# Kernel optimization log

Hardware: AMD Instinct MI355X
Metric: run time of the kernel (lower is better)

Reference implementation:

```python
import jax, jax.numpy as jnp
import numpy as np

NUM_NODES = 100000
NUM_EDGES = 1600000
NUM_GRAPHS = 64
D_IN = 128
HID = 256
N_ATTR = 8
D_OUT = 1


def setup_inputs() -> dict:
    key = jax.random.key(0)
    ks = jax.random.split(key, 16)
    x = jax.random.normal(ks[0], (NUM_NODES, D_IN), dtype=jnp.float32)
    edge_index = jax.random.randint(ks[1], (2, NUM_EDGES), 0, NUM_NODES, dtype=jnp.int64)
    batch = jnp.sort(jax.random.randint(ks[2], (NUM_NODES,), 0, NUM_GRAPHS, dtype=jnp.int64))
    graph_attr = jax.random.normal(ks[3], (NUM_GRAPHS, N_ATTR), dtype=jnp.float32)
    def lin(k, fi, fo):
        s = 1.0 / np.sqrt(fi)
        return jax.random.uniform(k, (fi, fo), jnp.float32, -s, s)
    # SAGEConv: lin_l (applied to aggregated neighbors, has bias) + lin_r (root, no bias)
    W1l = lin(ks[4], D_IN, HID); b1 = jnp.zeros((HID,), jnp.float32)
    W1r = lin(ks[5], D_IN, HID)
    W2l = lin(ks[6], HID, HID); b2 = jnp.zeros((HID,), jnp.float32)
    W2r = lin(ks[7], HID, HID)
    Wf1 = lin(ks[8], HID + N_ATTR, HID); bf1 = jnp.zeros((HID,), jnp.float32)
    Wf2 = lin(ks[9], HID, D_OUT); bf2 = jnp.zeros((D_OUT,), jnp.float32)
    return {"x": x, "edge_index": edge_index, "batch": batch, "graph_attr": graph_attr,
            "W1l": W1l, "b1": b1, "W1r": W1r, "W2l": W2l, "b2": b2, "W2r": W2r,
            "Wf1": Wf1, "bf1": bf1, "Wf2": Wf2, "bf2": bf2}


def _mean_agg(h, src, dst, num_segments):
    # gather source features, scatter-mean into destination nodes
    s = jax.ops.segment_sum(h[src], dst, num_segments=num_segments)
    cnt = jax.ops.segment_sum(jnp.ones((src.shape[0], 1), h.dtype), dst, num_segments=num_segments)
    return s / jnp.maximum(cnt, 1.0)


def _sage(h, src, dst, Wl, b, Wr):
    agg = _mean_agg(h, src, dst, h.shape[0])
    return agg @ Wl + b + h @ Wr


def reference(x, edge_index, batch, graph_attr, W1l, b1, W1r, W2l, b2, W2r, Wf1, bf1, Wf2, bf2):
    src, dst = edge_index[0], edge_index[1]
    h = jax.nn.relu(_sage(x, src, dst, W1l, b1, W1r))
    h = _sage(h, src, dst, W2l, b2, W2r)
    # global mean pool over graphs
    gsum = jax.ops.segment_sum(h, batch, num_segments=NUM_GRAPHS)
    gcnt = jax.ops.segment_sum(jnp.ones((h.shape[0], 1), h.dtype), batch, num_segments=NUM_GRAPHS)
    g = gsum / jnp.maximum(gcnt, 1.0)
    g = jnp.concatenate([g, graph_attr.reshape(-1, N_ATTR)], axis=1)
    g = jax.nn.relu(g @ Wf1 + bf1)
    return g @ Wf2 + bf2
```

## Files before the change

kernel.cpp:

```cpp
#include <hip/hip_runtime.h>
#include <stdint.h>

#define NN 100000
#define NE 1600000
#define NG 64
#define DIN 128
#define HID 256
#define NATTR 8
#define NBK 391
#define CAP 6144
#define PCH 4096
#define BWW 25000

typedef unsigned short u16;
typedef __attribute__((ext_vector_type(8))) short s16x8;
typedef __attribute__((ext_vector_type(4))) float f32x4;

__device__ __forceinline__ int imaxi(int a, int b) { return a > b ? a : b; }
__device__ __forceinline__ u16 f2bf(float f) {
    unsigned u = __float_as_uint(f);
    unsigned r = (u + 0x7fffu + ((u >> 16) & 1u)) >> 16;
    return (u16)r;
}


__global__ void k_init(float4* __restrict__ P84, const int* __restrict__ batch,
                       int* __restrict__ goff, int* __restrict__ gcnt,
                       int* __restrict__ cursor) {
    if (blockIdx.x < 256) {
        int i = blockIdx.x * 256 + threadIdx.x;
        if (i < 8 * 128 * HID / 4) P84[i] = make_float4(0.f, 0.f, 0.f, 0.f);
    } else {
        int g = threadIdx.x;
        for (int i = g; i < NBK; i += 256) cursor[i] = 0;
        if (g <= NG) {
            int lo = 0, hi = NN;
            while (lo < hi) {
                int mid = (lo + hi) >> 1;
                if (batch[mid] < g) lo = mid + 1; else hi = mid;
            }
            goff[g] = lo;
        }
        __syncthreads();
        if (g < NG) gcnt[g] = goff[g + 1] - goff[g];
    }
}


#define CB 12756

__global__ void k_prep(const float4* __restrict__ x4, ushort4* __restrict__ xb4,
                       const float* __restrict__ W1l, const float* __restrict__ W1r,
                       u16* __restrict__ W1lt, u16* __restrict__ W1rt) {
    int i = blockIdx.x * 256 + threadIdx.x;
    const int NX4 = NN * DIN / 4;
    if (i < NX4) {
        float4 v = x4[i];
        ushort4 o;
        o.x = f2bf(v.x); o.y = f2bf(v.y); o.z = f2bf(v.z); o.w = f2bf(v.w);
        xb4[i] = o;
    } else {
        int j = i - NX4;
        if (j < 32768) {
            int n = j >> 7, k = j & 127;
            W1lt[j] = f2bf(W1l[k * HID + n]);
        } else if (j < 65536) {
            int jj = j - 32768;
            int n = jj >> 7, k = jj & 127;
            W1rt[jj] = f2bf(W1r[k * HID + n]);
        }
    }
}


__global__ __launch_bounds__(256) void k_part(const int* __restrict__ ei,
                                              int* __restrict__ cursor,
                                              uint2* __restrict__ pairs) {
    __shared__ unsigned sdst[PCH];
    __shared__ unsigned ssrc[PCH];
    __shared__ int hist[NBK];
    __shared__ int sc[512];
    __shared__ int gb[NBK];
    int t = threadIdx.x;
    int c0 = blockIdx.x * PCH;
    int n = NE - c0; if (n > PCH) n = PCH;
    for (int i = t; i < NBK; i += 256) hist[i] = 0;
    __syncthreads();
    unsigned mydst[16], mysrc[16];
    int myoff[16];
#pragma unroll
    for (int j = 0; j < 16; j++) {
        int i = t + j * 256;
        myoff[j] = -1;
        if (i < n) {
            int e = c0 + i;
            mydst[j] = (unsigned)__builtin_nontemporal_load(&ei[NE + e]);
            mysrc[j] = (unsigned)__builtin_nontemporal_load(&ei[e]);
            myoff[j] = atomicAdd(&hist[mydst[j] >> 8], 1);
        }
    }
    __syncthreads();
    sc[t] = (t < NBK) ? hist[t] : 0;
    sc[t + 256] = (t + 256 < NBK) ? hist[t + 256] : 0;
    __syncthreads();
    for (int off = 1; off < 512; off <<= 1) {
        int v0 = (t >= off) ? sc[t - off] : 0;
        int v1 = (t + 256 >= off) ? sc[t + 256 - off] : 0;
        __syncthreads();
        sc[t] += v0; sc[t + 256] += v1;
        __syncthreads();
    }
    if (t < NBK && hist[t] > 0) gb[t] = atomicAdd(&cursor[t], hist[t]);
    if (t + 256 < NBK && hist[t + 256] > 0)
        gb[t + 256] = atomicAdd(&cursor[t + 256], hist[t + 256]);
    __syncthreads();
#pragma unroll
    for (int j = 0; j < 16; j++) {
        if (myoff[j] >= 0) {
            int b = mydst[j] >> 8;
            int pos = sc[b] - hist[b] + myoff[j];
            sdst[pos] = mydst[j];
            ssrc[pos] = mysrc[j];
        }
    }
    __syncthreads();
    for (int i = t; i < n; i += 256) {
        unsigned d = sdst[i];
        int b = d >> 8;
        int local = gb[b] + (i - (sc[b] - hist[b]));
        pairs[(size_t)b * CAP + local] = make_uint2(ssrc[i], d);
    }
}


__global__ void k_bscan(const int* __restrict__ cursor, int* __restrict__ ebase) {
    __shared__ int sc[512];
    int t = threadIdx.x;
    sc[t] = (t < NBK) ? cursor[t] : 0;
    sc[t + 256] = (t + 256 < NBK) ? cursor[t + 256] : 0;
    __syncthreads();
    for (int off = 1; off < 512; off <<= 1) {
        int v0 = (t >= off) ? sc[t - off] : 0;
        int v1 = (t + 256 >= off) ? sc[t + 256 - off] : 0;
        __syncthreads();
        sc[t] += v0; sc[t + 256] += v1;
        __syncthreads();
    }
    if (t < NBK) ebase[t] = sc[t] - cursor[t];
    if (t + 256 < NBK) ebase[t + 256] = sc[t + 256] - cursor[t + 256];
    if (t == 0) ebase[NBK] = sc[NBK - 1];
}


__global__ __launch_bounds__(256) void k_csr(const uint2* __restrict__ pairs,
                                             const int* __restrict__ cursor,
                                             const int* __restrict__ ebase,
                                             int* __restrict__ rowptr,
                                             unsigned* __restrict__ col) {
    __shared__ unsigned colL[CAP];
    __shared__ int cnt[256], cur[256], sc[256];
    int b = blockIdx.x, t = threadIdx.x;
    int nb0 = b << 8;
    int ecnt = cursor[b];
    int obase = ebase[b];
    const uint2* pp = pairs + (size_t)b * CAP;
    cnt[t] = 0;
    __syncthreads();
    for (int i = t; i < ecnt; i += 256)
        atomicAdd(&cnt[pp[i].y & 255], 1);
    __syncthreads();
    sc[t] = cnt[t];
    __syncthreads();
    for (int off = 1; off < 256; off <<= 1) {
        int v = (t >= off) ? sc[t - off] : 0;
        __syncthreads();
        sc[t] += v;
        __syncthreads();
    }
    int lr = sc[t] - cnt[t];
    cur[t] = lr;
    int node = nb0 + t;
    if (node < NN) rowptr[node] = obase + lr;
    if (b == NBK - 1 && t == 0) rowptr[NN] = obase + ecnt;
    __syncthreads();
    for (int i = t; i < ecnt; i += 256) {
        uint2 p = pp[i];
        int dl = p.y & 255;
        int pos = atomicAdd(&cur[dl], 1);
        int dd = cnt[dl]; if (dd > 32767) dd = 32767;
        colL[pos] = ((unsigned)dd << 17) | p.x;
    }
    __syncthreads();
    for (int i = t; i < ecnt; i += 256)
        col[obase + i] = colL[i];
}


__global__ void k_agg(const uint2* __restrict__ xb2, uint2* __restrict__ agg2,
                      const int* __restrict__ rowptr, const unsigned* __restrict__ col) {
    int node = blockIdx.x * 4 + (threadIdx.x >> 6);
    int lane = threadIdx.x & 63;
    if (node >= NN) return;
    int half = lane >> 5, li = lane & 31;
    int s = rowptr[node], e = rowptr[node + 1];
    float a0 = 0.f, a1 = 0.f, a2 = 0.f, a3 = 0.f;
    int i = s + half;
    for (; i + 6 < e; i += 8) {
        unsigned u0 = col[i] & 0x1FFFFu, u1 = col[i + 2] & 0x1FFFFu;
        unsigned u2 = col[i + 4] & 0x1FFFFu, u3 = col[i + 6] & 0x1FFFFu;
        uint2 w0 = xb2[(size_t)u0 * 32 + li];
        uint2 w1 = xb2[(size_t)u1 * 32 + li];
        uint2 w2 = xb2[(size_t)u2 * 32 + li];
        uint2 w3 = xb2[(size_t)u3 * 32 + li];
        a0 += __uint_as_float(w0.x << 16); a1 += __uint_as_float(w0.x & 0xffff0000u);
        a2 += __uint_as_float(w0.y << 16); a3 += __uint_as_float(w0.y & 0xffff0000u);
        a0 += __uint_as_float(w1.x << 16); a1 += __uint_as_float(w1.x & 0xffff0000u);
        a2 += __uint_as_float(w1.y << 16); a3 += __uint_as_float(w1.y & 0xffff0000u);
        a0 += __uint_as_float(w2.x << 16); a1 += __uint_as_float(w2.x & 0xffff0000u);
        a2 += __uint_as_float(w2.y << 16); a3 += __uint_as_float(w2.y & 0xffff0000u);
        a0 += __uint_as_float(w3.x << 16); a1 += __uint_as_float(w3.x & 0xffff0000u);
        a2 += __uint_as_float(w3.y << 16); a3 += __uint_as_float(w3.y & 0xffff0000u);
    }
    for (; i < e; i += 2) {
        unsigned u = col[i] & 0x1FFFFu;
        uint2 w = xb2[(size_t)u * 32 + li];
        a0 += __uint_as_float(w.x << 16); a1 += __uint_as_float(w.x & 0xffff0000u);
        a2 += __uint_as_float(w.y << 16); a3 += __uint_as_float(w.y & 0xffff0000u);
    }
    a0 += __shfl_xor(a0, 32); a1 += __shfl_xor(a1, 32);
    a2 += __shfl_xor(a2, 32); a3 += __shfl_xor(a3, 32);
    if (half == 0) {
        float inv = 1.f / (float)imaxi(e - s, 1);
        uint2 o;
        o.x = (((unsigned)f2bf(a1 * inv)) << 16) | (unsigned)f2bf(a0 * inv);
        o.y = (((unsigned)f2bf(a3 * inv)) << 16) | (unsigned)f2bf(a2 * inv);
        agg2[(size_t)node * 32 + li] = o;
    }
}


__global__ __launch_bounds__(256) void k_gemm1(
    const u16* __restrict__ agg1, const u16* __restrict__ xb,
    const u16* __restrict__ W1lt, const u16* __restrict__ W1rt,
    const float* __restrict__ b1, u16* __restrict__ h1t) {
    __shared__ u16 As[128][40];
    __shared__ u16 Bs[128][40];
    int t = threadIdx.x;
    int m0 = blockIdx.x * 128;
    int n0 = blockIdx.y * 128;
    int wave = t >> 6, lane = t & 63;
    int wm = wave & 1, wn = wave >> 1;
    int lm = lane & 15, quad = lane >> 4;
    f32x4 acc[4][4] = {};
    const u16* Ap = agg1;
    const u16* Bp = W1lt;
#pragma unroll
    for (int ph = 0; ph < 2; ph++) {
        for (int k0 = 0; k0 < DIN; k0 += 32) {
#pragma unroll
            for (int i = 0; i < 2; i++) {
                int flat = t + i * 256;
                int r = flat >> 2, q = flat & 3;
                int m = m0 + r;
                uint4 v = {0u, 0u, 0u, 0u};
                if (m < NN) v = *(const uint4*)(Ap + (size_t)m * DIN + k0 + q * 8);
                *(uint4*)&As[r][q * 8] = v;
                uint4 w = *(const uint4*)(Bp + (size_t)(n0 + r) * DIN + k0 + q * 8);
                *(uint4*)&Bs[r][q * 8] = w;
            }
            __syncthreads();
            s16x8 af[4], bfr[4];
#pragma unroll
            for (int i = 0; i < 4; i++) {
                af[i]  = *(const s16x8*)&As[wm * 64 + i * 16 + lm][quad * 8];
                bfr[i] = *(const s16x8*)&Bs[wn * 64 + i * 16 + lm][quad * 8];
            }
#pragma unroll
            for (int mi = 0; mi < 4; mi++)
#pragma unroll
                for (int ni = 0; ni < 4; ni++)
                    acc[mi][ni] = __builtin_amdgcn_mfma_f32_16x16x32_bf16(
                        af[mi], bfr[ni], acc[mi][ni], 0, 0, 0);
            __syncthreads();
        }
        Ap = xb; Bp = W1rt;
    }
#pragma unroll
    for (int ni = 0; ni < 4; ni++) {
        int colf = n0 + wn * 64 + ni * 16 + lm;
        float bias = b1[colf];
#pragma unroll
        for (int mi = 0; mi < 4; mi++) {
            int row = m0 + wm * 64 + mi * 16 + quad * 4;
            if (row < NN) {
                ushort4 o;
                o.x = f2bf(fmaxf(acc[mi][ni][0] + bias, 0.f));
                o.y = f2bf(fmaxf(acc[mi][ni][1] + bias, 0.f));
                o.z = f2bf(fmaxf(acc[mi][ni][2] + bias, 0.f));
                o.w = f2bf(fmaxf(acc[mi][ni][3] + bias, 0.f));
                *(ushort4*)(h1t + (size_t)colf * NN + row) = o;
            }
        }
    }
}


__global__ __launch_bounds__(256) void k_bw(
    const int* __restrict__ rowptr, const unsigned* __restrict__ col,
    const int* __restrict__ goff, u16* __restrict__ Wbt) {
    int b = blockIdx.x;
    int t = threadIdx.x;
    if (b < 256) {
        __shared__ float bins[BWW];
        int g = b >> 2, w = b & 3;
        int lo = w * BWW;
        for (int i = t; i < BWW; i += 256) bins[i] = 0.f;
        __syncthreads();
        int ebeg = rowptr[goff[g]], eend = rowptr[goff[g + 1]];
        for (int i = ebeg + t; i < eend; i += 256) {
            unsigned c = col[i];
            unsigned sl = (c & 0x1FFFFu) - lo;
            if (sl < (unsigned)BWW) atomicAdd(&bins[sl], 1.0f / (float)(c >> 17));
        }
        __syncthreads();
        u16* out = Wbt + (size_t)g * NN + lo;
        for (int k = t; k < BWW / 4; k += 256) {
            ushort4 o;
            o.x = f2bf(bins[4 * k + 0]); o.y = f2bf(bins[4 * k + 1]);
            o.z = f2bf(bins[4 * k + 2]); o.w = f2bf(bins[4 * k + 3]);
            *(ushort4*)(out + 4 * k) = o;
        }
    } else {
        int g = b - 256;
        int a = goff[g], bnd = goff[g + 1];
        u16* out = Wbt + (size_t)(NG + g) * NN;
        for (int k = t; k < NN / 4; k += 256) {
            int c0 = 4 * k;
            ushort4 o;
            o.x = (c0 + 0 >= a && c0 + 0 < bnd) ? 0x3F80 : 0;
            o.y = (c0 + 1 >= a && c0 + 1 < bnd) ? 0x3F80 : 0;
            o.z = (c0 + 2 >= a && c0 + 2 < bnd) ? 0x3F80 : 0;
            o.w = (c0 + 3 >= a && c0 + 3 < bnd) ? 0x3F80 : 0;
            *(ushort4*)(out + c0) = o;
        }
    }
}


#define KCHUNK 1024

__global__ __launch_bounds__(256) void k_poolg(
    const u16* __restrict__ Wbt, const u16* __restrict__ h1t, float* __restrict__ P8) {
    __shared__ u16 As[128][40];
    __shared__ u16 Bs[128][40];
    int t = threadIdx.x;
    int kbase = blockIdx.x * KCHUNK;
    int n0 = blockIdx.y * 128;
    int krem = NN - kbase;
    int ksteps = (krem < KCHUNK ? krem : KCHUNK) >> 5;
    int wave = t >> 6, lane = t & 63;
    int wm = wave & 1, wn = wave >> 1;
    int lm = lane & 15, quad = lane >> 4;
    float* P = P8 + (size_t)(blockIdx.x & 7) * 128 * HID;
    f32x4 acc[4][4] = {};
    for (int ks = 0; ks < ksteps; ks++) {
        int k0 = kbase + ks * 32;
#pragma unroll
        for (int i = 0; i < 2; i++) {
            int flat = t + i * 256;
            int r = flat >> 2, q = flat & 3;
            uint4 v = *(const uint4*)(Wbt + (size_t)r * NN + k0 + q * 8);
            *(uint4*)&As[r][q * 8] = v;
            uint4 w = *(const uint4*)(h1t + (size_t)(n0 + r) * NN + k0 + q * 8);
            *(uint4*)&Bs[r][q * 8] = w;
        }
        __syncthreads();
        s16x8 af[4], bfr[4];
#pragma unroll
        for (int i = 0; i < 4; i++) {
            af[i]  = *(const s16x8*)&As[wm * 64 + i * 16 + lm][quad * 8];
            bfr[i] = *(const s16x8*)&Bs[wn * 64 + i * 16 + lm][quad * 8];
        }
#pragma unroll
        for (int mi = 0; mi < 4; mi++)
#pragma unroll
            for (int ni = 0; ni < 4; ni++)
                acc[mi][ni] = __builtin_amdgcn_mfma_f32_16x16x32_bf16(
                    af[mi], bfr[ni], acc[mi][ni], 0, 0, 0);
        __syncthreads();
    }
#pragma unroll
    for (int mi = 0; mi < 4; mi++)
#pragma unroll
        for (int ni = 0; ni < 4; ni++) {
            int gcol = wm * 64 + mi * 16 + quad * 4;
            int feat = n0 + wn * 64 + ni * 16 + lm;
#pragma unroll
            for (int r = 0; r < 4; r++)
                atomicAdd(&P[(gcol + r) * HID + feat], acc[mi][ni][r]);
        }
}


__global__ void k_head(const float* __restrict__ P8, const int* __restrict__ gcnt,
                       const float* __restrict__ gattr,
                       const float* __restrict__ W2l, const float* __restrict__ b2,
                       const float* __restrict__ W2r,
                       const float* __restrict__ Wf1, const float* __restrict__ bf1,
                       const float* __restrict__ Wf2, const float* __restrict__ bf2v,
                       float* __restrict__ out) {
    __shared__ float pa[HID], ph[HID], gv[HID + NATTR];
    __shared__ float red[256];
    int g = blockIdx.x, t = threadIdx.x;
    float sa = 0.f, sh = 0.f;
#pragma unroll
    for (int c = 0; c < 8; c++) {
        sa += P8[(size_t)c * 128 * HID + g * HID + t];
        sh += P8[(size_t)c * 128 * HID + (NG + g) * HID + t];
    }
    pa[t] = sa; ph[t] = sh;
    __syncthreads();
    float s = 0.f;
    for (int k = 0; k < HID; k++)
        s += pa[k] * W2l[k * HID + t] + ph[k] * W2r[k * HID + t];
    float invc = 1.f / (float)imaxi(gcnt[g], 1);
    gv[t] = s * invc + b2[t];
    if (t < NATTR) gv[HID + t] = gattr[g * NATTR + t];
    __syncthreads();
    float h = bf1[t];
    for (int k = 0; k < HID + NATTR; k++) h += gv[k] * Wf1[k * HID + t];
    h = fmaxf(h, 0.f);
    red[t] = h * Wf2[t];
    __syncthreads();
    for (int off = 128; off > 0; off >>= 1) {
        if (t < off) red[t] += red[t + off];
        __syncthreads();
    }
    if (t == 0) out[g] = red[0] + bf2v[0];
}


extern "C" void kernel_launch(void* const* d_in, const int* in_sizes, int n_in,
                              void* d_out, int out_size, void* d_ws, size_t ws_size,
                              hipStream_t stream) {
    (void)in_sizes; (void)n_in; (void)out_size; (void)ws_size;
    const float* x     = (const float*)d_in[0];
    const int*   ei    = (const int*)d_in[1];
    const int*   batch = (const int*)d_in[2];
    const float* gattr = (const float*)d_in[3];
    const float* W1l   = (const float*)d_in[4];
    const float* b1    = (const float*)d_in[5];
    const float* W1r   = (const float*)d_in[6];
    const float* W2l   = (const float*)d_in[7];
    const float* b2    = (const float*)d_in[8];
    const float* W2r   = (const float*)d_in[9];
    const float* Wf1   = (const float*)d_in[10];
    const float* bf1   = (const float*)d_in[11];
    const float* Wf2   = (const float*)d_in[12];
    const float* bf2v  = (const float*)d_in[13];
    float* out = (float*)d_out;

    uint8_t* w = (uint8_t*)d_ws;
    size_t off = 0;
    auto alloc = [&](size_t bytes) -> void* {
        void* p = w + off;
        off += (bytes + 255) & ~(size_t)255;
        return p;
    };
    u16*      xb     = (u16*)alloc((size_t)NN * DIN * 2);
    u16*      agg1   = (u16*)alloc((size_t)NN * DIN * 2);
    u16*      h1t    = (u16*)alloc((size_t)NN * HID * 2);
    u16*      Wbt    = (u16*)alloc((size_t)128 * NN * 2);
    u16*      W1lt   = (u16*)alloc((size_t)HID * DIN * 2);
    u16*      W1rt   = (u16*)alloc((size_t)HID * DIN * 2);
    uint2*    pairs  = (uint2*)alloc((size_t)NBK * CAP * 8);
    int*      rowptr = (int*)alloc((size_t)(NN + 1) * 4);
    unsigned* col    = (unsigned*)alloc((size_t)NE * 4);
    int*      cursor = (int*)alloc((NBK + 1) * 4);
    int*      ebase  = (int*)alloc((NBK + 1) * 4);
    int*      goff   = (int*)alloc((NG + 1) * 4);
    int*      gcnt   = (int*)alloc(NG * 4);
    float*    P8     = (float*)alloc((size_t)8 * 128 * HID * 4);

    k_init<<<257, 256, 0, stream>>>((float4*)P8, batch, goff, gcnt, cursor);
    k_prep<<<CB, 256, 0, stream>>>((const float4*)x, (ushort4*)xb, W1l, W1r, W1lt, W1rt);

    k_part<<<(NE + PCH - 1) / PCH, 256, 0, stream>>>(ei, cursor, pairs);
    k_bscan<<<1, 256, 0, stream>>>(cursor, ebase);
    k_csr<<<NBK, 256, 0, stream>>>(pairs, cursor, ebase, rowptr, col);

    k_agg<<<NN / 4, 256, 0, stream>>>((const uint2*)xb, (uint2*)agg1, rowptr, col);
    dim3 g1((NN + 127) / 128, HID / 128);
    k_gemm1<<<g1, 256, 0, stream>>>(agg1, xb, W1lt, W1rt, b1, h1t);

    k_bw<<<320, 256, 0, stream>>>(rowptr, col, goff, Wbt);
    dim3 g2((NN + KCHUNK - 1) / KCHUNK, HID / 128);
    k_poolg<<<g2, 256, 0, stream>>>(Wbt, h1t, P8);

    k_head<<<NG, 256, 0, stream>>>(P8, gcnt, gattr, W2l, b2, W2r, Wf1, bf1, Wf2, bf2v, out);
}
```

Baseline: 388.6 us.

## Merge init/prep and bscan kernels, pack edge pairs, widen gathers, use direct-to-LDS loads

Merges k_init into k_prep and folds the bucket scan into k_csr, which removes two launches. Edge pairs are packed into one 32-bit word, halving partition traffic. k_agg now gathers 16-byte vectors per lane and uses quarter-wave edge parallelism. The GEMMs move to 512-thread blocks covering all 256 output features, use global_load_lds without padding, and pooling uses smaller K chunks. Risks: the unpadded LDS layout may cause bank conflicts, the gemm1 tail has no M bounds guard, and every k_csr block repeats the redundant scan.

```diff
diff --git a/kernel.cpp b/kernel.cpp
--- a/kernel.cpp
+++ b/kernel.cpp
@@ -11,6 +11,7 @@
 #define CAP 6144
 #define PCH 4096
 #define BWW 25000
+#define CB 12756
 
 typedef unsigned short u16;
 typedef __attribute__((ext_vector_type(8))) short s16x8;
@@ -19,20 +20,46 @@
 __device__ __forceinline__ int imaxi(int a, int b) { return a > b ? a : b; }
 __device__ __forceinline__ u16 f2bf(float f) {
     unsigned u = __float_as_uint(f);
-    unsigned r = (u + 0x7fffu + ((u >> 16) & 1u)) >> 16;
-    return (u16)r;
-}
-
-
-__global__ void k_init(float4* __restrict__ P84, const int* __restrict__ batch,
+    return (u16)((u + 0x7fffu + ((u >> 16) & 1u)) >> 16);
+}
+__device__ __forceinline__ void gload16(const void* g, void* l) {
+    __builtin_amdgcn_global_load_lds((const __attribute__((address_space(1))) void*)g,
+                                     (__attribute__((address_space(3))) void*)l, 16, 0, 0);
+}
+
+
+__global__ void k_prep(const float4* __restrict__ x4, ushort4* __restrict__ xb4,
+                       const float* __restrict__ W1l, const float* __restrict__ W1r,
+                       u16* __restrict__ W1lt, u16* __restrict__ W1rt,
+                       float4* __restrict__ P84, const int* __restrict__ batch,
                        int* __restrict__ goff, int* __restrict__ gcnt,
                        int* __restrict__ cursor) {
-    if (blockIdx.x < 256) {
-        int i = blockIdx.x * 256 + threadIdx.x;
-        if (i < 8 * 128 * HID / 4) P84[i] = make_float4(0.f, 0.f, 0.f, 0.f);
+    int b = blockIdx.x, t = threadIdx.x;
+    if (b < CB) {
+        int i = b * 256 + t;
+        const int NX4 = NN * DIN / 4;
+        if (i < NX4) {
+            float4 v = x4[i];
+            ushort4 o;
+            o.x = f2bf(v.x); o.y = f2bf(v.y); o.z = f2bf(v.z); o.w = f2bf(v.w);
+            xb4[i] = o;
+        } else {
+            int j = i - NX4;
+            if (j < 32768) {
+                int n = j >> 7, k = j & 127;
+                W1lt[j] = f2bf(W1l[k * HID + n]);
+            } else if (j < 65536) {
+                int jj = j - 32768;
+                int n = jj >> 7, k = jj & 127;
+                W1rt[jj] = f2bf(W1r[k * HID + n]);
+            }
+        }
+    } else if (b < CB + 256) {
+        int i = (b - CB) * 256 + t;
+        P84[i] = make_float4(0.f, 0.f, 0.f, 0.f);
     } else {
-        int g = threadIdx.x;
-        for (int i = g; i < NBK; i += 256) cursor[i] = 0;
+        for (int i = t; i < NBK; i += 256) cursor[i] = 0;
+        int g = t;
         if (g <= NG) {
             int lo = 0, hi = NN;
             while (lo < hi) {
@@ -47,56 +74,31 @@
 }
 
 
-#define CB 12756
-
-__global__ void k_prep(const float4* __restrict__ x4, ushort4* __restrict__ xb4,
-                       const float* __restrict__ W1l, const float* __restrict__ W1r,
-                       u16* __restrict__ W1lt, u16* __restrict__ W1rt) {
-    int i = blockIdx.x * 256 + threadIdx.x;
-    const int NX4 = NN * DIN / 4;
-    if (i < NX4) {
-        float4 v = x4[i];
-        ushort4 o;
-        o.x = f2bf(v.x); o.y = f2bf(v.y); o.z = f2bf(v.z); o.w = f2bf(v.w);
-        xb4[i] = o;
-    } else {
-        int j = i - NX4;
-        if (j < 32768) {
-            int n = j >> 7, k = j & 127;
-            W1lt[j] = f2bf(W1l[k * HID + n]);
-        } else if (j < 65536) {
-            int jj = j - 32768;
-            int n = jj >> 7, k = jj & 127;
-            W1rt[jj] = f2bf(W1r[k * HID + n]);
-        }
-    }
-}
-
-
 __global__ __launch_bounds__(256) void k_part(const int* __restrict__ ei,
                                               int* __restrict__ cursor,
-                                              uint2* __restrict__ pairs) {
-    __shared__ unsigned sdst[PCH];
-    __shared__ unsigned ssrc[PCH];
-    __shared__ int hist[NBK];
+                                              unsigned* __restrict__ pairs) {
+    __shared__ unsigned spk[PCH];
+    __shared__ unsigned short sbk[PCH];
+    __shared__ int hist[NBK], gb[NBK];
     __shared__ int sc[512];
-    __shared__ int gb[NBK];
     int t = threadIdx.x;
     int c0 = blockIdx.x * PCH;
     int n = NE - c0; if (n > PCH) n = PCH;
     for (int i = t; i < NBK; i += 256) hist[i] = 0;
     __syncthreads();
-    unsigned mydst[16], mysrc[16];
-    int myoff[16];
+    unsigned mypk[16]; unsigned short mybk[16]; int myoff[16];
 #pragma unroll
     for (int j = 0; j < 16; j++) {
         int i = t + j * 256;
         myoff[j] = -1;
         if (i < n) {
             int e = c0 + i;
-            mydst[j] = (unsigned)__builtin_nontemporal_load(&ei[NE + e]);
-            mysrc[j] = (unsigned)__builtin_nontemporal_load(&ei[e]);
-            myoff[j] = atomicAdd(&hist[mydst[j] >> 8], 1);
+            unsigned d = (unsigned)__builtin_nontemporal_load(&ei[NE + e]);
+            unsigned s = (unsigned)__builtin_nontemporal_load(&ei[e]);
+            unsigned bk = d >> 8;
+            mypk[j] = ((d & 255u) << 24) | s;
+            mybk[j] = (unsigned short)bk;
+            myoff[j] = atomicAdd(&hist[bk], 1);
         }
     }
     __syncthreads();
@@ -117,57 +119,46 @@
 #pragma unroll
     for (int j = 0; j < 16; j++) {
         if (myoff[j] >= 0) {
-            int b = mydst[j] >> 8;
-            int pos = sc[b] - hist[b] + myoff[j];
-            sdst[pos] = mydst[j];
-            ssrc[pos] = mysrc[j];
+            int bk = mybk[j];
+            int pos = sc[bk] - hist[bk] + myoff[j];
+            spk[pos] = mypk[j];
+            sbk[pos] = (unsigned short)bk;
         }
     }
     __syncthreads();
     for (int i = t; i < n; i += 256) {
-        unsigned d = sdst[i];
-        int b = d >> 8;
-        int local = gb[b] + (i - (sc[b] - hist[b]));
-        pairs[(size_t)b * CAP + local] = make_uint2(ssrc[i], d);
-    }
-}
-
-
-__global__ void k_bscan(const int* __restrict__ cursor, int* __restrict__ ebase) {
-    __shared__ int sc[512];
-    int t = threadIdx.x;
-    sc[t] = (t < NBK) ? cursor[t] : 0;
-    sc[t + 256] = (t + 256 < NBK) ? cursor[t + 256] : 0;
-    __syncthreads();
-    for (int off = 1; off < 512; off <<= 1) {
-        int v0 = (t >= off) ? sc[t - off] : 0;
-        int v1 = (t + 256 >= off) ? sc[t + 256 - off] : 0;
-        __syncthreads();
-        sc[t] += v0; sc[t + 256] += v1;
-        __syncthreads();
-    }
-    if (t < NBK) ebase[t] = sc[t] - cursor[t];
-    if (t + 256 < NBK) ebase[t + 256] = sc[t + 256] - cursor[t + 256];
-    if (t == 0) ebase[NBK] = sc[NBK - 1];
-}
-
-
-__global__ __launch_bounds__(256) void k_csr(const uint2* __restrict__ pairs,
+        int bk = sbk[i];
+        int local = gb[bk] + (i - (sc[bk] - hist[bk]));
+        pairs[(size_t)bk * CAP + local] = spk[i];
+    }
+}
+
+
+__global__ __launch_bounds__(256) void k_csr(const unsigned* __restrict__ pairs,
                                              const int* __restrict__ cursor,
-                                             const int* __restrict__ ebase,
                                              int* __restrict__ rowptr,
                                              unsigned* __restrict__ col) {
     __shared__ unsigned colL[CAP];
+    __shared__ int csc[512];
     __shared__ int cnt[256], cur[256], sc[256];
     int b = blockIdx.x, t = threadIdx.x;
-    int nb0 = b << 8;
+    csc[t] = (t < NBK) ? cursor[t] : 0;
+    csc[t + 256] = (t + 256 < NBK) ? cursor[t + 256] : 0;
+    __syncthreads();
+    for (int off = 1; off < 512; off <<= 1) {
+        int v0 = (t >= off) ? csc[t - off] : 0;
+        int v1 = (t + 256 >= off) ? csc[t + 256 - off] : 0;
+        __syncthreads();
+        csc[t] += v0; csc[t + 256] += v1;
+        __syncthreads();
+    }
+    int obase = (b == 0) ? 0 : csc[b - 1];
     int ecnt = cursor[b];
-    int obase = ebase[b];
-    const uint2* pp = pairs + (size_t)b * CAP;
+    const unsigned* pp = pairs + (size_t)b * CAP;
     cnt[t] = 0;
     __syncthreads();
     for (int i = t; i < ecnt; i += 256)
-        atomicAdd(&cnt[pp[i].y & 255], 1);
+        atomicAdd(&cnt[pp[i] >> 24], 1);
     __syncthreads();
     sc[t] = cnt[t];
     __syncthreads();
@@ -179,16 +170,16 @@
     }
     int lr = sc[t] - cnt[t];
     cur[t] = lr;
-    int node = nb0 + t;
+    int node = (b << 8) + t;
     if (node < NN) rowptr[node] = obase + lr;
     if (b == NBK - 1 && t == 0) rowptr[NN] = obase + ecnt;
     __syncthreads();
     for (int i = t; i < ecnt; i += 256) {
-        uint2 p = pp[i];
-        int dl = p.y & 255;
+        unsigned p = pp[i];
+        int dl = p >> 24;
         int pos = atomicAdd(&cur[dl], 1);
         int dd = cnt[dl]; if (dd > 32767) dd = 32767;
-        colL[pos] = ((unsigned)dd << 17) | p.x;
+        colL[pos] = ((unsigned)dd << 17) | (p & 0xFFFFFFu);
     }
     __syncthreads();
     for (int i = t; i < ecnt; i += 256)
@@ -196,77 +187,85 @@
 }
 
 
-__global__ void k_agg(const uint2* __restrict__ xb2, uint2* __restrict__ agg2,
+__global__ void k_agg(const uint4* __restrict__ xb4, uint4* __restrict__ agg4,
                       const int* __restrict__ rowptr, const unsigned* __restrict__ col) {
     int node = blockIdx.x * 4 + (threadIdx.x >> 6);
     int lane = threadIdx.x & 63;
     if (node >= NN) return;
-    int half = lane >> 5, li = lane & 31;
+    int qtr = lane >> 4, li = lane & 15;
     int s = rowptr[node], e = rowptr[node + 1];
-    float a0 = 0.f, a1 = 0.f, a2 = 0.f, a3 = 0.f;
-    int i = s + half;
-    for (; i + 6 < e; i += 8) {
-        unsigned u0 = col[i] & 0x1FFFFu, u1 = col[i + 2] & 0x1FFFFu;
-        unsigned u2 = col[i + 4] & 0x1FFFFu, u3 = col[i + 6] & 0x1FFFFu;
-        uint2 w0 = xb2[(size_t)u0 * 32 + li];
-        uint2 w1 = xb2[(size_t)u1 * 32 + li];
-        uint2 w2 = xb2[(size_t)u2 * 32 + li];
-        uint2 w3 = xb2[(size_t)u3 * 32 + li];
-        a0 += __uint_as_float(w0.x << 16); a1 += __uint_as_float(w0.x & 0xffff0000u);
-        a2 += __uint_as_float(w0.y << 16); a3 += __uint_as_float(w0.y & 0xffff0000u);
-        a0 += __uint_as_float(w1.x << 16); a1 += __uint_as_float(w1.x & 0xffff0000u);
-        a2 += __uint_as_float(w1.y << 16); a3 += __uint_as_float(w1.y & 0xffff0000u);
-        a0 += __uint_as_float(w2.x << 16); a1 += __uint_as_float(w2.x & 0xffff0000u);
-        a2 += __uint_as_float(w2.y << 16); a3 += __uint_as_float(w2.y & 0xffff0000u);
-        a0 += __uint_as_float(w3.x << 16); a1 += __uint_as_float(w3.x & 0xffff0000u);
-        a2 += __uint_as_float(w3.y << 16); a3 += __uint_as_float(w3.y & 0xffff0000u);
-    }
-    for (; i < e; i += 2) {
-        unsigned u = col[i] & 0x1FFFFu;
-        uint2 w = xb2[(size_t)u * 32 + li];
-        a0 += __uint_as_float(w.x << 16); a1 += __uint_as_float(w.x & 0xffff0000u);
-        a2 += __uint_as_float(w.y << 16); a3 += __uint_as_float(w.y & 0xffff0000u);
-    }
+    float a0 = 0, a1 = 0, a2 = 0, a3 = 0, a4 = 0, a5 = 0, a6 = 0, a7 = 0;
+#define ACC8(V) do { \
+        a0 += __uint_as_float((V).x << 16); a1 += __uint_as_float((V).x & 0xffff0000u); \
+        a2 += __uint_as_float((V).y << 16); a3 += __uint_as_float((V).y & 0xffff0000u); \
+        a4 += __uint_as_float((V).z << 16); a5 += __uint_as_float((V).z & 0xffff0000u); \
+        a6 += __uint_as_float((V).w << 16); a7 += __uint_as_float((V).w & 0xffff0000u); } while (0)
+    int i = s;
+    for (; i + 16 <= e; i += 16) {
+        unsigned c0 = col[i + qtr] & 0x1FFFFu;
+        unsigned c1 = col[i + 4 + qtr] & 0x1FFFFu;
+        unsigned c2 = col[i + 8 + qtr] & 0x1FFFFu;
+        unsigned c3 = col[i + 12 + qtr] & 0x1FFFFu;
+        uint4 w0 = xb4[(size_t)c0 * 16 + li];
+        uint4 w1 = xb4[(size_t)c1 * 16 + li];
+        uint4 w2 = xb4[(size_t)c2 * 16 + li];
+        uint4 w3 = xb4[(size_t)c3 * 16 + li];
+        ACC8(w0); ACC8(w1); ACC8(w2); ACC8(w3);
+    }
+    for (; i + 4 <= e; i += 4) {
+        unsigned c = col[i + qtr] & 0x1FFFFu;
+        uint4 wv = xb4[(size_t)c * 16 + li];
+        ACC8(wv);
+    }
+    if (i + qtr < e) {
+        unsigned c = col[i + qtr] & 0x1FFFFu;
+        uint4 wv = xb4[(size_t)c * 16 + li];
+        ACC8(wv);
+    }
+#undef ACC8
+    a0 += __shfl_xor(a0, 16); a1 += __shfl_xor(a1, 16);
+    a2 += __shfl_xor(a2, 16); a3 += __shfl_xor(a3, 16);
+    a4 += __shfl_xor(a4, 16); a5 += __shfl_xor(a5, 16);
+    a6 += __shfl_xor(a6, 16); a7 += __shfl_xor(a7, 16);
     a0 += __shfl_xor(a0, 32); a1 += __shfl_xor(a1, 32);
     a2 += __shfl_xor(a2, 32); a3 += __shfl_xor(a3, 32);
-    if (half == 0) {
+    a4 += __shfl_xor(a4, 32); a5 += __shfl_xor(a5, 32);
+    a6 += __shfl_xor(a6, 32); a7 += __shfl_xor(a7, 32);
+    if (qtr == 0) {
         float inv = 1.f / (float)imaxi(e - s, 1);
-        uint2 o;
+        uint4 o;
         o.x = (((unsigned)f2bf(a1 * inv)) << 16) | (unsigned)f2bf(a0 * inv);
         o.y = (((unsigned)f2bf(a3 * inv)) << 16) | (unsigned)f2bf(a2 * inv);
-        agg2[(size_t)node * 32 + li] = o;
-    }
-}
-
-
-__global__ __launch_bounds__(256) void k_gemm1(
+        o.z = (((unsigned)f2bf(a5 * inv)) << 16) | (unsigned)f2bf(a4 * inv);
+        o.w = (((unsigned)f2bf(a7 * inv)) << 16) | (unsigned)f2bf(a6 * inv);
+        agg4[(size_t)node * 16 + li] = o;
+    }
+}
+
+
+__global__ __launch_bounds__(512) void k_gemm1(
     const u16* __restrict__ agg1, const u16* __restrict__ xb,
     const u16* __restrict__ W1lt, const u16* __restrict__ W1rt,
     const float* __restrict__ b1, u16* __restrict__ h1t) {
-    __shared__ u16 As[128][40];
-    __shared__ u16 Bs[128][40];
+    __shared__ u16 As[128][32];
+    __shared__ u16 Bs[256][32];
     int t = threadIdx.x;
     int m0 = blockIdx.x * 128;
-    int n0 = blockIdx.y * 128;
     int wave = t >> 6, lane = t & 63;
     int wm = wave & 1, wn = wave >> 1;
     int lm = lane & 15, quad = lane >> 4;
+    int ar = t >> 2, aq = t & 3;
     f32x4 acc[4][4] = {};
     const u16* Ap = agg1;
     const u16* Bp = W1lt;
 #pragma unroll
     for (int ph = 0; ph < 2; ph++) {
         for (int k0 = 0; k0 < DIN; k0 += 32) {
+            gload16(Ap + (size_t)(m0 + ar) * DIN + k0 + aq * 8, &As[wave * 16][0]);
 #pragma unroll
             for (int i = 0; i < 2; i++) {
-                int flat = t + i * 256;
-                int r = flat >> 2, q = flat & 3;
-                int m = m0 + r;
-                uint4 v = {0u, 0u, 0u, 0u};
-                if (m < NN) v = *(const uint4*)(Ap + (size_t)m * DIN + k0 + q * 8);
-                *(uint4*)&As[r][q * 8] = v;
-                uint4 w = *(const uint4*)(Bp + (size_t)(n0 + r) * DIN + k0 + q * 8);
-                *(uint4*)&Bs[r][q * 8] = w;
+                int r = (t + i * 512) >> 2;
+                gload16(Bp + (size_t)r * DIN + k0 + aq * 8, &Bs[wave * 16 + i * 128][0]);
             }
             __syncthreads();
             s16x8 af[4], bfr[4];
@@ -287,7 +286,7 @@
     }
 #pragma unroll
     for (int ni = 0; ni < 4; ni++) {
-        int colf = n0 + wn * 64 + ni * 16 + lm;
+        int colf = wn * 64 + ni * 16 + lm;
         float bias = b1[colf];
 #pragma unroll
         for (int mi = 0; mi < 4; mi++) {
@@ -308,8 +307,7 @@
 __global__ __launch_bounds__(256) void k_bw(
     const int* __restrict__ rowptr, const unsigned* __restrict__ col,
     const int* __restrict__ goff, u16* __restrict__ Wbt) {
-    int b = blockIdx.x;
-    int t = threadIdx.x;
+    int b = blockIdx.x, t = threadIdx.x;
     if (b < 256) {
         __shared__ float bins[BWW];
         int g = b >> 2, w = b & 3;
@@ -347,32 +345,29 @@
 }
 
 
-#define KCHUNK 1024
-
-__global__ __launch_bounds__(256) void k_poolg(
+#define KCHUNK 512
+
+__global__ __launch_bounds__(512) void k_poolg(
     const u16* __restrict__ Wbt, const u16* __restrict__ h1t, float* __restrict__ P8) {
-    __shared__ u16 As[128][40];
-    __shared__ u16 Bs[128][40];
+    __shared__ u16 As[128][32];
+    __shared__ u16 Bs[256][32];
     int t = threadIdx.x;
     int kbase = blockIdx.x * KCHUNK;
-    int n0 = blockIdx.y * 128;
     int krem = NN - kbase;
     int ksteps = (krem < KCHUNK ? krem : KCHUNK) >> 5;
     int wave = t >> 6, lane = t & 63;
     int wm = wave & 1, wn = wave >> 1;
     int lm = lane & 15, quad = lane >> 4;
+    int ar = t >> 2, aq = t & 3;
     float* P = P8 + (size_t)(blockIdx.x & 7) * 128 * HID;
     f32x4 acc[4][4] = {};
     for (int ks = 0; ks < ksteps; ks++) {
         int k0 = kbase + ks * 32;
+        gload16(Wbt + (size_t)ar * NN + k0 + aq * 8, &As[wave * 16][0]);
 #pragma unroll
         for (int i = 0; i < 2; i++) {
-            int flat = t + i * 256;
-            int r = flat >> 2, q = flat & 3;
-            uint4 v = *(const uint4*)(Wbt + (size_t)r * NN + k0 + q * 8);
-            *(uint4*)&As[r][q * 8] = v;
-            uint4 w = *(const uint4*)(h1t + (size_t)(n0 + r) * NN + k0 + q * 8);
-            *(uint4*)&Bs[r][q * 8] = w;
+            int r = (t + i * 512) >> 2;
+            gload16(h1t + (size_t)r * NN + k0 + aq * 8, &Bs[wave * 16 + i * 128][0]);
         }
         __syncthreads();
         s16x8 af[4], bfr[4];
@@ -394,7 +389,7 @@
 #pragma unroll
         for (int ni = 0; ni < 4; ni++) {
             int gcol = wm * 64 + mi * 16 + quad * 4;
-            int feat = n0 + wn * 64 + ni * 16 + lm;
+            int feat = wn * 64 + ni * 16 + lm;
 #pragma unroll
             for (int r = 0; r < 4; r++)
                 atomicAdd(&P[(gcol + r) * HID + feat], acc[mi][ni][r]);
@@ -473,29 +468,26 @@
     u16*      Wbt    = (u16*)alloc((size_t)128 * NN * 2);
     u16*      W1lt   = (u16*)alloc((size_t)HID * DIN * 2);
     u16*      W1rt   = (u16*)alloc((size_t)HID * DIN * 2);
-    uint2*    pairs  = (uint2*)alloc((size_t)NBK * CAP * 8);
+    unsigned* pairs  = (unsigned*)alloc((size_t)NBK * CAP * 4);
     int*      rowptr = (int*)alloc((size_t)(NN + 1) * 4);
     unsigned* col    = (unsigned*)alloc((size_t)NE * 4);
     int*      cursor = (int*)alloc((NBK + 1) * 4);
-    int*      ebase  = (int*)alloc((NBK + 1) * 4);
     int*      goff   = (int*)alloc((NG + 1) * 4);
     int*      gcnt   = (int*)alloc(NG * 4);
     float*    P8     = (float*)alloc((size_t)8 * 128 * HID * 4);
 
-    k_init<<<257, 256, 0, stream>>>((float4*)P8, batch, goff, gcnt, cursor);
-    k_prep<<<CB, 256, 0, stream>>>((const float4*)x, (ushort4*)xb, W1l, W1r, W1lt, W1rt);
+    k_prep<<<CB + 257, 256, 0, stream>>>((const float4*)x, (ushort4*)xb, W1l, W1r,
+                                         W1lt, W1rt, (float4*)P8, batch, goff, gcnt,
+                                         cursor);
 
     k_part<<<(NE + PCH - 1) / PCH, 256, 0, stream>>>(ei, cursor, pairs);
-    k_bscan<<<1, 256, 0, stream>>>(cursor, ebase);
-    k_csr<<<NBK, 256, 0, stream>>>(pairs, cursor, ebase, rowptr, col);
-
-    k_agg<<<NN / 4, 256, 0, stream>>>((const uint2*)xb, (uint2*)agg1, rowptr, col);
-    dim3 g1((NN + 127) / 128, HID / 128);
-    k_gemm1<<<g1, 256, 0, stream>>>(agg1, xb, W1lt, W1rt, b1, h1t);
+    k_csr<<<NBK, 256, 0, stream>>>(pairs, cursor, rowptr, col);
+
+    k_agg<<<NN / 4, 256, 0, stream>>>((const uint4*)xb, (uint4*)agg1, rowptr, col);
+    k_gemm1<<<(NN + 127) / 128, 512, 0, stream>>>(agg1, xb, W1lt, W1rt, b1, h1t);
 
     k_bw<<<320, 256, 0, stream>>>(rowptr, col, goff, Wbt);
-    dim3 g2((NN + KCHUNK - 1) / KCHUNK, HID / 128);
-    k_poolg<<<g2, 256, 0, stream>>>(Wbt, h1t, P8);
+    k_poolg<<<(NN + KCHUNK - 1) / KCHUNK, 512, 0, stream>>>(Wbt, h1t, P8);
 
     k_head<<<NG, 256, 0, stream>>>(P8, gcnt, gattr, W2l, b2, W2r, Wf1, bf1, Wf2, bf2v, out);
 }
```

Result: faster. 367.7 us (-5.4%).
